# Performance work log

Measured on AMD Instinct MI355X. Metric: run time of the kernel, lower is better.

## Reference

```python
import jax, jax.numpy as jnp
import numpy as np

NEG_SLOPE = 0.2
LN_EPS = 1e-5


def _gat_layer(x, src, dst, W, a_src, a_dst, N):
    # x: [N, Fin], W: [Fin, H*C], a_src/a_dst: [H, C]
    H, C = a_src.shape
    h = (x @ W).reshape(N, H, C)
    al_src = (h * a_src).sum(-1)  # [N, H]
    al_dst = (h * a_dst).sum(-1)  # [N, H]
    e = jax.nn.leaky_relu(al_src[src] + al_dst[dst], NEG_SLOPE)  # [E, H]
    m = jax.ops.segment_max(e, dst, num_segments=N)
    e = jnp.exp(e - m[dst])
    denom = jax.ops.segment_sum(e, dst, num_segments=N)
    alpha = e / denom[dst]  # softmax over incoming edges per dst node
    msg = h[src] * alpha[:, :, None]  # [E, H, C]
    return jax.ops.segment_sum(msg, dst, num_segments=N)  # [N, H, C]


def _layer_norm(x, g, b):
    mu = x.mean(-1, keepdims=True)
    var = ((x - mu) ** 2).mean(-1, keepdims=True)
    return (x - mu) * jax.lax.rsqrt(var + LN_EPS) * g + b


def setup_inputs() -> dict:
    key = jax.random.key(0)
    ks = jax.random.split(key, 20)
    N, E, Fin, Ch, H = 50000, 800000, 128, 64, 4
    s = lambda k, shp, sc=0.05: jax.random.normal(k, shp, dtype=jnp.float32) * sc
    return {
        "x": jax.random.normal(ks[0], (N, Fin), dtype=jnp.float32),
        "edge_index": jax.random.randint(ks[1], (2, E), 0, N, dtype=jnp.int64),
        "W1": s(ks[2], (Fin, H * Ch)),
        "att_src1": s(ks[3], (H, Ch)),
        "att_dst1": s(ks[4], (H, Ch)),
        "b1": jnp.zeros((H * Ch,), jnp.float32),
        "ln1_g": jnp.ones((H * Ch,), jnp.float32),
        "ln1_b": jnp.zeros((H * Ch,), jnp.float32),
        "W2": s(ks[5], (H * Ch, Ch)),
        "att_src2": s(ks[6], (1, Ch)),
        "att_dst2": s(ks[7], (1, Ch)),
        "b2": jnp.zeros((Ch,), jnp.float32),
        "ln2_g": jnp.ones((Ch,), jnp.float32),
        "ln2_b": jnp.zeros((Ch,), jnp.float32),
        "fc1_W": s(ks[8], (Ch, Ch // 2)),
        "fc1_b": jnp.zeros((Ch // 2,), jnp.float32),
        "fc2_W": s(ks[9], (Ch // 2, 1)),
        "fc2_b": jnp.zeros((1,), jnp.float32),
    }


def reference(x, edge_index, W1, att_src1, att_dst1, b1, ln1_g, ln1_b,
              W2, att_src2, att_dst2, b2, ln2_g, ln2_b,
              fc1_W, fc1_b, fc2_W, fc2_b):
    N = x.shape[0]
    # PyG GATConv adds self-loops by default
    loop = jnp.arange(N, dtype=edge_index.dtype)
    src = jnp.concatenate([edge_index[0], loop])
    dst = jnp.concatenate([edge_index[1], loop])

    # GAT layer 1 (heads=4, concat) + LayerNorm + ReLU (dropout is identity in eval)
    h = _gat_layer(x, src, dst, W1, att_src1, att_dst1, N).reshape(N, -1) + b1
    h = jax.nn.relu(_layer_norm(h, ln1_g, ln1_b))

    # GAT layer 2 (heads=1) + LayerNorm + ReLU
    h = _gat_layer(h, src, dst, W2, att_src2, att_dst2, N).reshape(N, -1) + b2
    h = jax.nn.relu(_layer_norm(h, ln2_g, ln2_b))

    # MLP head
    h = jax.nn.relu(h @ fc1_W + fc1_b)
    return h @ fc2_W + fc2_b  # [N, 1]
```

## Files before the change

### kernel.cpp

```cpp
#include <hip/hip_runtime.h>
#include <hip/hip_fp16.h>
#include <math.h>

#define NEG_SLOPE 0.2f
#define LN_EPS 1e-5f
#define SCCHUNK 8192
#define PADCAP 64
#define CURPAD 32

typedef __attribute__((ext_vector_type(8))) _Float16 half8;
typedef __attribute__((ext_vector_type(4))) _Float16 half4;
typedef __attribute__((ext_vector_type(4))) float floatx4;

static __device__ __forceinline__ float lrelu(float e) {
    return e > 0.0f ? e : NEG_SLOPE * e;
}

__global__ __launch_bounds__(256) void k_g1sc(
    const float* __restrict__ x, const float* __restrict__ W1,
    const float* __restrict__ as1, const float* __restrict__ ad1,
    _Float16* __restrict__ h1, float* __restrict__ als, float* __restrict__ ald,
    const int* __restrict__ ei, unsigned* __restrict__ cursor,
    unsigned short* __restrict__ eidx,
    int N, int E, int nsc)
{
    const int tid = threadIdx.x;

    if ((int)blockIdx.x < nsc) {
        const unsigned basev = cursor[(size_t)N * CURPAD];
        const int Et = E + N;
        const int i0 = blockIdx.x * SCCHUNK;
#pragma unroll 4
        for (int j = 0; j < SCCHUNK / 256; ++j) {
            int i = i0 + j * 256 + tid;
            if (i < Et) {
                int s, d;
                if (i < E) { s = ei[i]; d = ei[E + i]; } else { s = d = i - E; }
                unsigned pos = atomicAdd(&cursor[(size_t)d * CURPAD], 1u) - basev;
                if (pos < PADCAP) eidx[(size_t)d * PADCAP + pos] = (unsigned short)s;
            }
        }
        return;
    }

    const int tile = blockIdx.x - nsc;
    const int lane = tid & 63, w = tid >> 6;
    const int l15 = lane & 15, quad = lane >> 4;
    const int r_base = tile * 64;

    half8 B[4][4];
    float asv[4], adv[4];
#pragma unroll
    for (int nt = 0; nt < 4; ++nt) {
        const int n = w * 64 + nt * 16 + l15;
        asv[nt] = as1[n]; adv[nt] = ad1[n];
#pragma unroll
        for (int ks = 0; ks < 4; ++ks) {
            const int k0 = ks * 32 + quad * 8;
            half8 b;
#pragma unroll
            for (int j = 0; j < 8; ++j) b[j] = (_Float16)W1[(size_t)(k0 + j) * 256 + n];
            B[ks][nt] = b;
        }
    }

#pragma unroll
    for (int rt = 0; rt < 4; ++rt) {
        const int r0 = r_base + rt * 16;
        int m = r0 + l15; if (m >= N) m = N - 1;
        half8 A[4];
#pragma unroll
        for (int ks = 0; ks < 4; ++ks) {
            const int k0 = ks * 32 + quad * 8;
            const float4* xp = (const float4*)(x + (size_t)m * 128 + k0);
            float4 v0 = xp[0], v1 = xp[1];
            half8 a;
            a[0] = (_Float16)v0.x; a[1] = (_Float16)v0.y; a[2] = (_Float16)v0.z; a[3] = (_Float16)v0.w;
            a[4] = (_Float16)v1.x; a[5] = (_Float16)v1.y; a[6] = (_Float16)v1.z; a[7] = (_Float16)v1.w;
            A[ks] = a;
        }
        floatx4 C[4];
#pragma unroll
        for (int nt = 0; nt < 4; ++nt) C[nt] = (floatx4){0.f, 0.f, 0.f, 0.f};
#pragma unroll
        for (int ks = 0; ks < 4; ++ks)
#pragma unroll
            for (int nt = 0; nt < 4; ++nt)
                C[nt] = __builtin_amdgcn_mfma_f32_16x16x32_f16(A[ks], B[ks][nt], C[nt], 0, 0, 0);

#pragma unroll
        for (int reg = 0; reg < 4; ++reg) {
            const int row = r0 + quad * 4 + reg;
            float vs = 0.f, vd = 0.f;
#pragma unroll
            for (int nt = 0; nt < 4; ++nt) {
                float c = C[nt][reg];
                if (row < N) h1[(size_t)row * 256 + w * 64 + nt * 16 + l15] = (_Float16)c;
                vs += c * asv[nt]; vd += c * adv[nt];
            }
#pragma unroll
            for (int o = 1; o < 16; o <<= 1) { vs += __shfl_xor(vs, o); vd += __shfl_xor(vd, o); }
            if (l15 == 0 && row < N) { als[row * 4 + w] = vs; ald[row * 4 + w] = vd; }
        }
    }
}

__global__ __launch_bounds__(256) void k_agg1(
    const _Float16* __restrict__ h1, const float* __restrict__ als, const float* __restrict__ ald,
    const unsigned* __restrict__ cursor, const unsigned short* __restrict__ eidx,
    const float* __restrict__ b1, const float* __restrict__ g1, const float* __restrict__ be1,
    _Float16* __restrict__ hln1, int N)
{
    __shared__ float alp[4][64][4];
    const int wv = threadIdx.x >> 6, lane = threadIdx.x & 63;
    int n = blockIdx.x * 4 + wv;
    if (n >= N) n = N - 1;
    const int base = n * PADCAP;
    const unsigned basev = cursor[(size_t)N * CURPAD];
    int deg = (int)(cursor[(size_t)n * CURPAD] - basev); if (deg > PADCAP) deg = PADCAP;
    const float4 ad = ((const float4*)ald)[n];

    const int srcv = eidx[base + (lane < deg ? lane : deg - 1)];
    float e0 = -1e30f, e1 = -1e30f, e2 = -1e30f, e3 = -1e30f;
    if (lane < deg) {
        float4 a4 = ((const float4*)als)[srcv];
        e0 = lrelu(a4.x + ad.x);
        e1 = lrelu(a4.y + ad.y);
        e2 = lrelu(a4.z + ad.z);
        e3 = lrelu(a4.w + ad.w);
    }
    float m0 = e0, m1 = e1, m2 = e2, m3 = e3;
#pragma unroll
    for (int o = 32; o; o >>= 1) {
        m0 = fmaxf(m0, __shfl_xor(m0, o));
        m1 = fmaxf(m1, __shfl_xor(m1, o));
        m2 = fmaxf(m2, __shfl_xor(m2, o));
        m3 = fmaxf(m3, __shfl_xor(m3, o));
    }
    float p0 = __expf(e0 - m0), p1 = __expf(e1 - m1);
    float p2 = __expf(e2 - m2), p3 = __expf(e3 - m3);
    float s0 = p0, s1 = p1, s2 = p2, s3 = p3;
#pragma unroll
    for (int o = 32; o; o >>= 1) {
        s0 += __shfl_xor(s0, o);
        s1 += __shfl_xor(s1, o);
        s2 += __shfl_xor(s2, o);
        s3 += __shfl_xor(s3, o);
    }
    float4 av;
    av.x = p0 / s0; av.y = p1 / s1; av.z = p2 / s2; av.w = p3 / s3;
    *(float4*)(&alp[wv][lane][0]) = av;

    float4 acc = make_float4(0.f, 0.f, 0.f, 0.f);
    const int hd = lane >> 4;
    const float* alpr = &alp[wv][0][hd];
    const int degr = (deg + 7) & ~7;
    for (int eb = 0; eb < degr; eb += 8) {
#pragma unroll
        for (int u = 0; u < 8; ++u) {
            const int e = eb + u;
            int s = __builtin_amdgcn_readlane(srcv, e);
            float a_e = alpr[e * 4];
            half4 v = *(const half4*)(h1 + (size_t)s * 256 + 4 * lane);
            acc.x = fmaf((float)v.x, a_e, acc.x);
            acc.y = fmaf((float)v.y, a_e, acc.y);
            acc.z = fmaf((float)v.z, a_e, acc.z);
            acc.w = fmaf((float)v.w, a_e, acc.w);
        }
    }

    float4 bb = ((const float4*)b1)[lane];
    float y0 = acc.x + bb.x, y1 = acc.y + bb.y, y2 = acc.z + bb.z, y3 = acc.w + bb.w;
    float ps = y0 + y1 + y2 + y3;
    float pss = y0 * y0 + y1 * y1 + y2 * y2 + y3 * y3;
#pragma unroll
    for (int o = 32; o; o >>= 1) { ps += __shfl_xor(ps, o); pss += __shfl_xor(pss, o); }
    float mu = ps * (1.f / 256.f);
    float var = pss * (1.f / 256.f) - mu * mu;
    float rstd = rsqrtf(var + LN_EPS);
    float4 gg = ((const float4*)g1)[lane];
    float4 b2v = ((const float4*)be1)[lane];
    half4 outv;
    outv.x = (_Float16)fmaxf((y0 - mu) * rstd * gg.x + b2v.x, 0.f);
    outv.y = (_Float16)fmaxf((y1 - mu) * rstd * gg.y + b2v.y, 0.f);
    outv.z = (_Float16)fmaxf((y2 - mu) * rstd * gg.z + b2v.z, 0.f);
    outv.w = (_Float16)fmaxf((y3 - mu) * rstd * gg.w + b2v.w, 0.f);
    ((half4*)(hln1 + (size_t)n * 256))[lane] = outv;
}

__global__ __launch_bounds__(256) void k_gemm2(
    const _Float16* __restrict__ hln1, const float* __restrict__ W2,
    const float* __restrict__ as2, const float* __restrict__ ad2,
    _Float16* __restrict__ h2, float* __restrict__ als2, float* __restrict__ ald2, int N)
{
    __shared__ float ps_s[4][64], ps_d[4][64];
    const int lane = threadIdx.x & 63, w = threadIdx.x >> 6;
    const int l15 = lane & 15, quad = lane >> 4;
    const int r_base = blockIdx.x * 64;

    const int n = w * 16 + l15;
    const float asv = as2[n], adv = ad2[n];
    half8 B[8];
#pragma unroll
    for (int ks = 0; ks < 8; ++ks) {
        const int k0 = ks * 32 + quad * 8;
        half8 b;
#pragma unroll
        for (int j = 0; j < 8; ++j) b[j] = (_Float16)W2[(size_t)(k0 + j) * 64 + n];
        B[ks] = b;
    }

#pragma unroll
    for (int rt = 0; rt < 4; ++rt) {
        const int r0 = r_base + rt * 16;
        int m = r0 + l15; if (m >= N) m = N - 1;
        floatx4 C = (floatx4){0.f, 0.f, 0.f, 0.f};
#pragma unroll
        for (int ks = 0; ks < 8; ++ks) {
            half8 a = *(const half8*)(hln1 + (size_t)m * 256 + ks * 32 + quad * 8);
            C = __builtin_amdgcn_mfma_f32_16x16x32_f16(a, B[ks], C, 0, 0, 0);
        }
#pragma unroll
        for (int reg = 0; reg < 4; ++reg) {
            const int row = r0 + quad * 4 + reg;
            float c = C[reg];
            if (row < N) h2[(size_t)row * 64 + n] = (_Float16)c;
            float vs = c * asv, vd = c * adv;
#pragma unroll
            for (int o = 1; o < 16; o <<= 1) { vs += __shfl_xor(vs, o); vd += __shfl_xor(vd, o); }
            if (l15 == 0) {
                ps_s[w][rt * 16 + quad * 4 + reg] = vs;
                ps_d[w][rt * 16 + quad * 4 + reg] = vd;
            }
        }
    }
    __syncthreads();
    const int t = threadIdx.x;
    if (t < 64) {
        const int row = r_base + t;
        if (row < N) {
            als2[row] = ps_s[0][t] + ps_s[1][t] + ps_s[2][t] + ps_s[3][t];
            ald2[row] = ps_d[0][t] + ps_d[1][t] + ps_d[2][t] + ps_d[3][t];
        }
    }
}

__global__ __launch_bounds__(256) void k_agg2(
    const _Float16* __restrict__ h2, const float* __restrict__ als, const float* __restrict__ ald,
    const unsigned* __restrict__ cursor, const unsigned short* __restrict__ eidx,
    const float* __restrict__ b2, const float* __restrict__ g2, const float* __restrict__ be2,
    const float* __restrict__ fc1W, const float* __restrict__ fc1b,
    const float* __restrict__ fc2W, const float* __restrict__ fc2b,
    float* __restrict__ out, int N)
{
    __shared__ float sh[4][64];
    const int wv = threadIdx.x >> 6, lane = threadIdx.x & 63;
    int n = blockIdx.x * 4 + wv;
    if (n >= N) n = N - 1;
    const int base = n * PADCAP;
    const unsigned basev = cursor[(size_t)N * CURPAD];
    int deg = (int)(cursor[(size_t)n * CURPAD] - basev); if (deg > PADCAP) deg = PADCAP;
    const float adn = ald[n];

    const int srcv = eidx[base + (lane < deg ? lane : deg - 1)];
    float e = -1e30f;
    if (lane < deg) e = lrelu(als[srcv] + adn);
    float m = e;
#pragma unroll
    for (int o = 32; o; o >>= 1) m = fmaxf(m, __shfl_xor(m, o));
    float p = __expf(e - m);
    float s = p;
#pragma unroll
    for (int o = 32; o; o >>= 1) s += __shfl_xor(s, o);
    const float alpha = p / s;

    float acc = 0.f;
    const int degr = (deg + 7) & ~7;
    for (int eb = 0; eb < degr; eb += 8) {
#pragma unroll
        for (int u = 0; u < 8; ++u) {
            const int e2 = eb + u;
            int sidx = __builtin_amdgcn_readlane(srcv, e2);
            float a_e = __int_as_float(
                __builtin_amdgcn_readlane(__float_as_int(alpha), e2));
            acc = fmaf((float)h2[(size_t)sidx * 64 + lane], a_e, acc);
        }
    }

    float y = acc + b2[lane];
    float ps = y, pss = y * y;
#pragma unroll
    for (int o = 32; o; o >>= 1) { ps += __shfl_xor(ps, o); pss += __shfl_xor(pss, o); }
    float mu = ps * (1.f / 64.f);
    float var = pss * (1.f / 64.f) - mu * mu;
    float r = fmaxf((y - mu) * rsqrtf(var + LN_EPS) * g2[lane] + be2[lane], 0.f);

    sh[wv][lane] = r;

    if (lane < 32) {
        float a1 = fc1b[lane];
#pragma unroll 8
        for (int k = 0; k < 64; ++k) a1 += sh[wv][k] * fc1W[k * 32 + lane];
        a1 = fmaxf(a1, 0.f);
        float t = a1 * fc2W[lane];
#pragma unroll
        for (int o = 16; o; o >>= 1) t += __shfl_xor(t, o);
        if (lane == 0) out[n] = t + fc2b[0];
    }
}

extern "C" void kernel_launch(void* const* d_in, const int* in_sizes, int n_in,
                              void* d_out, int out_size, void* d_ws, size_t ws_size,
                              hipStream_t stream)
{
    const float* x   = (const float*)d_in[0];
    const int* ei    = (const int*)d_in[1];
    const float* W1  = (const float*)d_in[2];
    const float* as1 = (const float*)d_in[3];
    const float* ad1 = (const float*)d_in[4];
    const float* b1  = (const float*)d_in[5];
    const float* g1  = (const float*)d_in[6];
    const float* be1 = (const float*)d_in[7];
    const float* W2  = (const float*)d_in[8];
    const float* as2 = (const float*)d_in[9];
    const float* ad2 = (const float*)d_in[10];
    const float* b2  = (const float*)d_in[11];
    const float* g2  = (const float*)d_in[12];
    const float* be2 = (const float*)d_in[13];
    const float* fc1W = (const float*)d_in[14];
    const float* fc1b = (const float*)d_in[15];
    const float* fc2W = (const float*)d_in[16];
    const float* fc2b = (const float*)d_in[17];
    float* out = (float*)d_out;

    const int N = in_sizes[0] / 128;
    const int E = in_sizes[1] / 2;
    const int Et = E + N;
    const int nsc = (Et + SCCHUNK - 1) / SCCHUNK;
    const int ntiles = (N + 63) / 64;

    char* p = (char*)d_ws;
    auto carve = [&](size_t bytes) {
        void* q = p;
        p += (bytes + 255) & ~(size_t)255;
        return q;
    };
    _Float16* h1    = (_Float16*)carve((size_t)N * 256 * 2);
    _Float16* hln1h = (_Float16*)carve((size_t)N * 256 * 2);
    _Float16* h2    = (_Float16*)carve((size_t)N * 64 * 2);
    float* als1 = (float*)carve((size_t)N * 4 * 4);
    float* ald1 = (float*)carve((size_t)N * 4 * 4);
    float* als2 = (float*)carve((size_t)N * 4);
    float* ald2 = (float*)carve((size_t)N * 4);
    unsigned* cursor = (unsigned*)carve((size_t)(N + 1) * CURPAD * 4);
    unsigned short* eidx = (unsigned short*)carve((size_t)N * PADCAP * 2);

    k_g1sc<<<nsc + ntiles, 256, 0, stream>>>(x, W1, as1, ad1, h1, als1, ald1,
                                             ei, cursor, eidx, N, E, nsc);
    k_agg1<<<(N + 3) / 4, 256, 0, stream>>>(h1, als1, ald1, cursor, eidx, b1, g1, be1, hln1h, N);
    k_gemm2<<<(N + 63) / 64, 256, 0, stream>>>(hln1h, W2, as2, ad2, h2, als2, ald2, N);
    k_agg2<<<(N + 3) / 4, 256, 0, stream>>>(h2, als2, ald2, cursor, eidx,
                                            b2, g2, be2, fc1W, fc1b, fc2W, fc2b, out, N);
}
```

Measured before the change: 277.4 us.

## Split fused scatter/GEMM1 kernel and batch scatter loads and atomics

The combined kernel that did edge scattering in some blocks and the layer-1 GEMM in others is split into two separate launches. The scatter kernel now loads all 32 edges per thread first, then issues all atomics, then all stores, so many memory operations are in flight at once instead of a serialized load-atomic-store chain. This costs an extra launch and loses the concurrent overlap of scatter and GEMM blocks within one grid, and it raises register pressure in the scatter kernel.

```diff
diff --git a/kernel.cpp b/kernel.cpp
--- a/kernel.cpp
+++ b/kernel.cpp
@@ -16,37 +16,52 @@
     return e > 0.0f ? e : NEG_SLOPE * e;
 }
 
-__global__ __launch_bounds__(256) void k_g1sc(
+__global__ __launch_bounds__(256) void k_scatter(
+    const int* __restrict__ ei, unsigned* __restrict__ cursor,
+    unsigned short* __restrict__ eidx, int N, int E)
+{
+    const int tid = threadIdx.x;
+    const unsigned basev = cursor[(size_t)N * CURPAD];
+    const int Et = E + N;
+    const int i0 = blockIdx.x * SCCHUNK;
+
+    int s[32], d[32];
+    unsigned pos[32];
+
+#pragma unroll
+    for (int j = 0; j < 32; ++j) {
+        const int i = i0 + j * 256 + tid;
+        if (i < Et) {
+            if (i < E) { s[j] = ei[i]; d[j] = ei[E + i]; }
+            else       { s[j] = d[j] = i - E; }
+        } else {
+            d[j] = -1;
+        }
+    }
+#pragma unroll
+    for (int j = 0; j < 32; ++j) {
+        if (d[j] >= 0)
+            pos[j] = atomicAdd(&cursor[(size_t)d[j] * CURPAD], 1u);
+    }
+#pragma unroll
+    for (int j = 0; j < 32; ++j) {
+        if (d[j] >= 0) {
+            unsigned p = pos[j] - basev;
+            if (p < PADCAP) eidx[(size_t)d[j] * PADCAP + p] = (unsigned short)s[j];
+        }
+    }
+}
+
+__global__ __launch_bounds__(256) void k_gemm1(
     const float* __restrict__ x, const float* __restrict__ W1,
     const float* __restrict__ as1, const float* __restrict__ ad1,
     _Float16* __restrict__ h1, float* __restrict__ als, float* __restrict__ ald,
-    const int* __restrict__ ei, unsigned* __restrict__ cursor,
-    unsigned short* __restrict__ eidx,
-    int N, int E, int nsc)
+    int N)
 {
     const int tid = threadIdx.x;
-
-    if ((int)blockIdx.x < nsc) {
-        const unsigned basev = cursor[(size_t)N * CURPAD];
-        const int Et = E + N;
-        const int i0 = blockIdx.x * SCCHUNK;
-#pragma unroll 4
-        for (int j = 0; j < SCCHUNK / 256; ++j) {
-            int i = i0 + j * 256 + tid;
-            if (i < Et) {
-                int s, d;
-                if (i < E) { s = ei[i]; d = ei[E + i]; } else { s = d = i - E; }
-                unsigned pos = atomicAdd(&cursor[(size_t)d * CURPAD], 1u) - basev;
-                if (pos < PADCAP) eidx[(size_t)d * PADCAP + pos] = (unsigned short)s;
-            }
-        }
-        return;
-    }
-
-    const int tile = blockIdx.x - nsc;
     const int lane = tid & 63, w = tid >> 6;
     const int l15 = lane & 15, quad = lane >> 4;
-    const int r_base = tile * 64;
+    const int r_base = blockIdx.x * 64;
 
     half8 B[4][4];
     float asv[4], adv[4];
@@ -355,8 +370,8 @@
     unsigned* cursor = (unsigned*)carve((size_t)(N + 1) * CURPAD * 4);
     unsigned short* eidx = (unsigned short*)carve((size_t)N * PADCAP * 2);
 
-    k_g1sc<<<nsc + ntiles, 256, 0, stream>>>(x, W1, as1, ad1, h1, als1, ald1,
-                                             ei, cursor, eidx, N, E, nsc);
+    k_scatter<<<nsc, 256, 0, stream>>>(ei, cursor, eidx, N, E);
+    k_gemm1<<<ntiles, 256, 0, stream>>>(x, W1, as1, ad1, h1, als1, ald1, N);
     k_agg1<<<(N + 3) / 4, 256, 0, stream>>>(h1, als1, ald1, cursor, eidx, b1, g1, be1, hln1h, N);
     k_gemm2<<<(N + 63) / 64, 256, 0, stream>>>(hln1h, W2, as2, ad2, h2, als2, ald2, N);
     k_agg2<<<(N + 3) / 4, 256, 0, stream>>>(h2, als2, ald2, cursor, eidx,
```

Result: slower. 307.1 us (+10.7%).

## Widen gather loads in GAT aggregation kernels, splitting edges across lane groups

Applied to the files above, without the earlier changes.

Both aggregation kernels now gather feature rows with wider per-lane loads: 16-byte half8 in layer 1 and half4 in layer 2. Each wave splits edges across lane groups (two halves or four quarters) and combines the partial sums with cross-lane shuffles. Source indices and attention weights are staged in shared memory and no longer broadcast with readlane. The aim is fewer, wider gather instructions and more edges in flight per iteration. The cost is extra shuffle reductions, shared-memory traffic, and the LayerNorm statistics being reduced over duplicated lanes (hence the adjusted divisors).

```diff
diff --git a/kernel.cpp b/kernel.cpp
--- a/kernel.cpp
+++ b/kernel.cpp
@@ -112,6 +112,7 @@
     _Float16* __restrict__ hln1, int N)
 {
     __shared__ float alp[4][64][4];
+    __shared__ int   srcl[4][64];
     const int wv = threadIdx.x >> 6, lane = threadIdx.x & 63;
     int n = blockIdx.x * 4 + wv;
     if (n >= N) n = N - 1;
@@ -150,42 +151,61 @@
     float4 av;
     av.x = p0 / s0; av.y = p1 / s1; av.z = p2 / s2; av.w = p3 / s3;
     *(float4*)(&alp[wv][lane][0]) = av;
-
-    float4 acc = make_float4(0.f, 0.f, 0.f, 0.f);
-    const int hd = lane >> 4;
-    const float* alpr = &alp[wv][0][hd];
+    srcl[wv][lane] = srcv;
+
+    const int half_ = lane >> 5, l31 = lane & 31, hd = l31 >> 3;
+    float4 a0 = make_float4(0.f, 0.f, 0.f, 0.f);
+    float4 a1 = make_float4(0.f, 0.f, 0.f, 0.f);
     const int degr = (deg + 7) & ~7;
     for (int eb = 0; eb < degr; eb += 8) {
 #pragma unroll
-        for (int u = 0; u < 8; ++u) {
-            const int e = eb + u;
-            int s = __builtin_amdgcn_readlane(srcv, e);
-            float a_e = alpr[e * 4];
-            half4 v = *(const half4*)(h1 + (size_t)s * 256 + 4 * lane);
-            acc.x = fmaf((float)v.x, a_e, acc.x);
-            acc.y = fmaf((float)v.y, a_e, acc.y);
-            acc.z = fmaf((float)v.z, a_e, acc.z);
-            acc.w = fmaf((float)v.w, a_e, acc.w);
-        }
-    }
-
-    float4 bb = ((const float4*)b1)[lane];
-    float y0 = acc.x + bb.x, y1 = acc.y + bb.y, y2 = acc.z + bb.z, y3 = acc.w + bb.w;
-    float ps = y0 + y1 + y2 + y3;
-    float pss = y0 * y0 + y1 * y1 + y2 * y2 + y3 * y3;
+        for (int u = 0; u < 4; ++u) {
+            const int e = eb + 2 * u + half_;
+            int s = srcl[wv][e];
+            float ae = alp[wv][e][hd];
+            half8 v = *(const half8*)(h1 + (size_t)s * 256 + l31 * 8);
+            a0.x = fmaf((float)v[0], ae, a0.x);
+            a0.y = fmaf((float)v[1], ae, a0.y);
+            a0.z = fmaf((float)v[2], ae, a0.z);
+            a0.w = fmaf((float)v[3], ae, a0.w);
+            a1.x = fmaf((float)v[4], ae, a1.x);
+            a1.y = fmaf((float)v[5], ae, a1.y);
+            a1.z = fmaf((float)v[6], ae, a1.z);
+            a1.w = fmaf((float)v[7], ae, a1.w);
+        }
+    }
+    a0.x += __shfl_xor(a0.x, 32); a0.y += __shfl_xor(a0.y, 32);
+    a0.z += __shfl_xor(a0.z, 32); a0.w += __shfl_xor(a0.w, 32);
+    a1.x += __shfl_xor(a1.x, 32); a1.y += __shfl_xor(a1.y, 32);
+    a1.z += __shfl_xor(a1.z, 32); a1.w += __shfl_xor(a1.w, 32);
+
+    const float4 bb0 = ((const float4*)b1)[l31 * 2];
+    const float4 bb1 = ((const float4*)b1)[l31 * 2 + 1];
+    float y0 = a0.x + bb0.x, y1 = a0.y + bb0.y, y2 = a0.z + bb0.z, y3 = a0.w + bb0.w;
+    float y4 = a1.x + bb1.x, y5 = a1.y + bb1.y, y6 = a1.z + bb1.z, y7 = a1.w + bb1.w;
+    float ps  = y0 + y1 + y2 + y3 + y4 + y5 + y6 + y7;
+    float pss = y0*y0 + y1*y1 + y2*y2 + y3*y3 + y4*y4 + y5*y5 + y6*y6 + y7*y7;
 #pragma unroll
     for (int o = 32; o; o >>= 1) { ps += __shfl_xor(ps, o); pss += __shfl_xor(pss, o); }
-    float mu = ps * (1.f / 256.f);
-    float var = pss * (1.f / 256.f) - mu * mu;
+    float mu = ps * (1.f / 512.f);
+    float var = pss * (1.f / 512.f) - mu * mu;
     float rstd = rsqrtf(var + LN_EPS);
-    float4 gg = ((const float4*)g1)[lane];
-    float4 b2v = ((const float4*)be1)[lane];
-    half4 outv;
-    outv.x = (_Float16)fmaxf((y0 - mu) * rstd * gg.x + b2v.x, 0.f);
-    outv.y = (_Float16)fmaxf((y1 - mu) * rstd * gg.y + b2v.y, 0.f);
-    outv.z = (_Float16)fmaxf((y2 - mu) * rstd * gg.z + b2v.z, 0.f);
-    outv.w = (_Float16)fmaxf((y3 - mu) * rstd * gg.w + b2v.w, 0.f);
-    ((half4*)(hln1 + (size_t)n * 256))[lane] = outv;
+    const float4 gg0 = ((const float4*)g1)[l31 * 2];
+    const float4 gg1 = ((const float4*)g1)[l31 * 2 + 1];
+    const float4 be0 = ((const float4*)be1)[l31 * 2];
+    const float4 be1v = ((const float4*)be1)[l31 * 2 + 1];
+    if (lane < 32) {
+        half8 outv;
+        outv[0] = (_Float16)fmaxf((y0 - mu) * rstd * gg0.x + be0.x, 0.f);
+        outv[1] = (_Float16)fmaxf((y1 - mu) * rstd * gg0.y + be0.y, 0.f);
+        outv[2] = (_Float16)fmaxf((y2 - mu) * rstd * gg0.z + be0.z, 0.f);
+        outv[3] = (_Float16)fmaxf((y3 - mu) * rstd * gg0.w + be0.w, 0.f);
+        outv[4] = (_Float16)fmaxf((y4 - mu) * rstd * gg1.x + be1v.x, 0.f);
+        outv[5] = (_Float16)fmaxf((y5 - mu) * rstd * gg1.y + be1v.y, 0.f);
+        outv[6] = (_Float16)fmaxf((y6 - mu) * rstd * gg1.z + be1v.z, 0.f);
+        outv[7] = (_Float16)fmaxf((y7 - mu) * rstd * gg1.w + be1v.w, 0.f);
+        *(half8*)(hln1 + (size_t)n * 256 + l31 * 8) = outv;
+    }
 }
 
 __global__ __launch_bounds__(256) void k_gemm2(
@@ -254,6 +274,8 @@
     float* __restrict__ out, int N)
 {
     __shared__ float sh[4][64];
+    __shared__ float alp2[4][64];
+    __shared__ int   src2[4][64];
     const int wv = threadIdx.x >> 6, lane = threadIdx.x & 63;
     int n = blockIdx.x * 4 + wv;
     if (n >= N) n = N - 1;
@@ -272,30 +294,49 @@
     float s = p;
 #pragma unroll
     for (int o = 32; o; o >>= 1) s += __shfl_xor(s, o);
-    const float alpha = p / s;
-
-    float acc = 0.f;
+    alp2[wv][lane] = p / s;
+    src2[wv][lane] = srcv;
+
+    const int grp = lane >> 4, l15 = lane & 15;
+    float4 acc = make_float4(0.f, 0.f, 0.f, 0.f);
     const int degr = (deg + 7) & ~7;
     for (int eb = 0; eb < degr; eb += 8) {
 #pragma unroll
-        for (int u = 0; u < 8; ++u) {
-            const int e2 = eb + u;
-            int sidx = __builtin_amdgcn_readlane(srcv, e2);
-            float a_e = __int_as_float(
-                __builtin_amdgcn_readlane(__float_as_int(alpha), e2));
-            acc = fmaf((float)h2[(size_t)sidx * 64 + lane], a_e, acc);
-        }
-    }
-
-    float y = acc + b2[lane];
-    float ps = y, pss = y * y;
+        for (int u = 0; u < 2; ++u) {
+            const int e2 = eb + 4 * u + grp;
+            int sidx = src2[wv][e2];
+            float a_e = alp2[wv][e2];
+            half4 v = *(const half4*)(h2 + (size_t)sidx * 64 + l15 * 4);
+            acc.x = fmaf((float)v.x, a_e, acc.x);
+            acc.y = fmaf((float)v.y, a_e, acc.y);
+            acc.z = fmaf((float)v.z, a_e, acc.z);
+            acc.w = fmaf((float)v.w, a_e, acc.w);
+        }
+    }
+    acc.x += __shfl_xor(acc.x, 16); acc.y += __shfl_xor(acc.y, 16);
+    acc.z += __shfl_xor(acc.z, 16); acc.w += __shfl_xor(acc.w, 16);
+    acc.x += __shfl_xor(acc.x, 32); acc.y += __shfl_xor(acc.y, 32);
+    acc.z += __shfl_xor(acc.z, 32); acc.w += __shfl_xor(acc.w, 32);
+
+    const float4 bb = ((const float4*)b2)[l15];
+    float y0 = acc.x + bb.x, y1 = acc.y + bb.y, y2 = acc.z + bb.z, y3 = acc.w + bb.w;
+    float ps = y0 + y1 + y2 + y3;
+    float pss = y0*y0 + y1*y1 + y2*y2 + y3*y3;
 #pragma unroll
     for (int o = 32; o; o >>= 1) { ps += __shfl_xor(ps, o); pss += __shfl_xor(pss, o); }
-    float mu = ps * (1.f / 64.f);
-    float var = pss * (1.f / 64.f) - mu * mu;
-    float r = fmaxf((y - mu) * rsqrtf(var + LN_EPS) * g2[lane] + be2[lane], 0.f);
-
-    sh[wv][lane] = r;
+    float mu = ps * (1.f / 256.f);
+    float var = pss * (1.f / 256.f) - mu * mu;
+    float rstd = rsqrtf(var + LN_EPS);
+    const float4 gg = ((const float4*)g2)[l15];
+    const float4 bev = ((const float4*)be2)[l15];
+    if (grp == 0) {
+        float4 r;
+        r.x = fmaxf((y0 - mu) * rstd * gg.x + bev.x, 0.f);
+        r.y = fmaxf((y1 - mu) * rstd * gg.y + bev.y, 0.f);
+        r.z = fmaxf((y2 - mu) * rstd * gg.z + bev.z, 0.f);
+        r.w = fmaxf((y3 - mu) * rstd * gg.w + bev.w, 0.f);
+        *(float4*)(&sh[wv][l15 * 4]) = r;
+    }
 
     if (lane < 32) {
         float a1 = fc1b[lane];
```

New measurement: 285.7 us. 3.0% more time.

## Fuse all four GAT stages into one persistent cooperative kernel with grid syncs

Applied to the files above, without the earlier changes.

Replaces the four separate kernel launches with a single cooperative persistent kernel. It uses grid-stride loops for the GEMM, aggregation and head stages, separated by grid.sync barriers. The aim is to remove launch overhead and inter-kernel gaps. In exchange, the grid is capped by occupancy (6 blocks/CU via launch bounds), which may reduce latency hiding in the memory-bound gather stages and adds grid-barrier cost.

```diff
diff --git a/kernel.cpp b/kernel.cpp
--- a/kernel.cpp
+++ b/kernel.cpp
@@ -1,6 +1,9 @@
 #include <hip/hip_runtime.h>
 #include <hip/hip_fp16.h>
+#include <hip/hip_cooperative_groups.h>
 #include <math.h>
+
+namespace cg = cooperative_groups;
 
 #define NEG_SLOPE 0.2f
 #define LN_EPS 1e-5f
@@ -16,20 +19,38 @@
     return e > 0.0f ? e : NEG_SLOPE * e;
 }
 
-__global__ __launch_bounds__(256) void k_g1sc(
-    const float* __restrict__ x, const float* __restrict__ W1,
-    const float* __restrict__ as1, const float* __restrict__ ad1,
-    _Float16* __restrict__ h1, float* __restrict__ als, float* __restrict__ ald,
-    const int* __restrict__ ei, unsigned* __restrict__ cursor,
-    unsigned short* __restrict__ eidx,
-    int N, int E, int nsc)
+__global__ __launch_bounds__(256, 6) void k_fused(
+    const float* __restrict__ x, const int* __restrict__ ei,
+    const float* __restrict__ W1, const float* __restrict__ as1, const float* __restrict__ ad1,
+    const float* __restrict__ b1, const float* __restrict__ g1, const float* __restrict__ be1,
+    const float* __restrict__ W2, const float* __restrict__ as2, const float* __restrict__ ad2,
+    const float* __restrict__ b2, const float* __restrict__ g2, const float* __restrict__ be2,
+    const float* __restrict__ fc1W, const float* __restrict__ fc1b,
+    const float* __restrict__ fc2W, const float* __restrict__ fc2b,
+    float* __restrict__ out,
+    _Float16* __restrict__ h1, _Float16* __restrict__ hln1, _Float16* __restrict__ h2,
+    float* __restrict__ als1, float* __restrict__ ald1,
+    float* __restrict__ als2, float* __restrict__ ald2,
+    unsigned* __restrict__ cursor, unsigned short* __restrict__ eidx,
+    int N, int E, int nsc, int ntiles, int nagg)
 {
+    cg::grid_group grid = cg::this_grid();
     const int tid = threadIdx.x;
-
-    if ((int)blockIdx.x < nsc) {
-        const unsigned basev = cursor[(size_t)N * CURPAD];
+    const int bid = blockIdx.x;
+    const int G = gridDim.x;
+    const int lane = tid & 63, wv = tid >> 6;
+    const int l15 = lane & 15, quad = lane >> 4;
+
+    __shared__ float s_alp[4][64][4];
+    __shared__ float s_ps[2][4][64];
+    __shared__ float s_sh[4][64];
+
+    const unsigned basev = cursor[(size_t)N * CURPAD];
+
+    if (bid >= G - nsc) {
+        const int chunk = bid - (G - nsc);
         const int Et = E + N;
-        const int i0 = blockIdx.x * SCCHUNK;
+        const int i0 = chunk * SCCHUNK;
 #pragma unroll 4
         for (int j = 0; j < SCCHUNK / 256; ++j) {
             int i = i0 + j * 256 + tid;
@@ -40,272 +61,246 @@
                 if (pos < PADCAP) eidx[(size_t)d * PADCAP + pos] = (unsigned short)s;
             }
         }
-        return;
-    }
-
-    const int tile = blockIdx.x - nsc;
-    const int lane = tid & 63, w = tid >> 6;
-    const int l15 = lane & 15, quad = lane >> 4;
-    const int r_base = tile * 64;
-
-    half8 B[4][4];
-    float asv[4], adv[4];
-#pragma unroll
-    for (int nt = 0; nt < 4; ++nt) {
-        const int n = w * 64 + nt * 16 + l15;
-        asv[nt] = as1[n]; adv[nt] = ad1[n];
-#pragma unroll
-        for (int ks = 0; ks < 4; ++ks) {
+    } else {
+        half8 B[4][4];
+        float asv[4], adv[4];
+#pragma unroll
+        for (int nt = 0; nt < 4; ++nt) {
+            const int n = wv * 64 + nt * 16 + l15;
+            asv[nt] = as1[n]; adv[nt] = ad1[n];
+#pragma unroll
+            for (int ks = 0; ks < 4; ++ks) {
+                const int k0 = ks * 32 + quad * 8;
+                half8 b;
+#pragma unroll
+                for (int j = 0; j < 8; ++j) b[j] = (_Float16)W1[(size_t)(k0 + j) * 256 + n];
+                B[ks][nt] = b;
+            }
+        }
+        for (int tile = bid; tile < ntiles; tile += (G - nsc)) {
+            const int r_base = tile * 64;
+#pragma unroll
+            for (int rt = 0; rt < 4; ++rt) {
+                const int r0 = r_base + rt * 16;
+                int m = r0 + l15; if (m >= N) m = N - 1;
+                half8 A[4];
+#pragma unroll
+                for (int ks = 0; ks < 4; ++ks) {
+                    const int k0 = ks * 32 + quad * 8;
+                    const float4* xp = (const float4*)(x + (size_t)m * 128 + k0);
+                    float4 v0 = xp[0], v1 = xp[1];
+                    half8 a;
+                    a[0] = (_Float16)v0.x; a[1] = (_Float16)v0.y; a[2] = (_Float16)v0.z; a[3] = (_Float16)v0.w;
+                    a[4] = (_Float16)v1.x; a[5] = (_Float16)v1.y; a[6] = (_Float16)v1.z; a[7] = (_Float16)v1.w;
+                    A[ks] = a;
+                }
+                floatx4 C[4];
+#pragma unroll
+                for (int nt = 0; nt < 4; ++nt) C[nt] = (floatx4){0.f, 0.f, 0.f, 0.f};
+#pragma unroll
+                for (int ks = 0; ks < 4; ++ks)
+#pragma unroll
+                    for (int nt = 0; nt < 4; ++nt)
+                        C[nt] = __builtin_amdgcn_mfma_f32_16x16x32_f16(A[ks], B[ks][nt], C[nt], 0, 0, 0);
+
+#pragma unroll
+                for (int reg = 0; reg < 4; ++reg) {
+                    const int row = r0 + quad * 4 + reg;
+                    float vs = 0.f, vd = 0.f;
+#pragma unroll
+                    for (int nt = 0; nt < 4; ++nt) {
+                        float c = C[nt][reg];
+                        if (row < N) h1[(size_t)row * 256 + wv * 64 + nt * 16 + l15] = (_Float16)c;
+                        vs += c * asv[nt]; vd += c * adv[nt];
+                    }
+#pragma unroll
+                    for (int o = 1; o < 16; o <<= 1) { vs += __shfl_xor(vs, o); vd += __shfl_xor(vd, o); }
+                    if (l15 == 0 && row < N) { als1[row * 4 + wv] = vs; ald1[row * 4 + wv] = vd; }
+                }
+            }
+        }
+    }
+    grid.sync();
+
+    for (int blk = bid; blk < nagg; blk += G) {
+        int n = blk * 4 + wv;
+        if (n >= N) n = N - 1;
+        const int base = n * PADCAP;
+        int deg = (int)(cursor[(size_t)n * CURPAD] - basev); if (deg > PADCAP) deg = PADCAP;
+        const float4 ad = ((const float4*)ald1)[n];
+
+        const int srcv = eidx[base + (lane < deg ? lane : deg - 1)];
+        float e0 = -1e30f, e1 = -1e30f, e2 = -1e30f, e3 = -1e30f;
+        if (lane < deg) {
+            float4 a4 = ((const float4*)als1)[srcv];
+            e0 = lrelu(a4.x + ad.x);
+            e1 = lrelu(a4.y + ad.y);
+            e2 = lrelu(a4.z + ad.z);
+            e3 = lrelu(a4.w + ad.w);
+        }
+        float m0 = e0, m1 = e1, m2 = e2, m3 = e3;
+#pragma unroll
+        for (int o = 32; o; o >>= 1) {
+            m0 = fmaxf(m0, __shfl_xor(m0, o));
+            m1 = fmaxf(m1, __shfl_xor(m1, o));
+            m2 = fmaxf(m2, __shfl_xor(m2, o));
+            m3 = fmaxf(m3, __shfl_xor(m3, o));
+        }
+        float p0 = __expf(e0 - m0), p1 = __expf(e1 - m1);
+        float p2 = __expf(e2 - m2), p3 = __expf(e3 - m3);
+        float s0 = p0, s1 = p1, s2 = p2, s3 = p3;
+#pragma unroll
+        for (int o = 32; o; o >>= 1) {
+            s0 += __shfl_xor(s0, o);
+            s1 += __shfl_xor(s1, o);
+            s2 += __shfl_xor(s2, o);
+            s3 += __shfl_xor(s3, o);
+        }
+        float4 av;
+        av.x = p0 / s0; av.y = p1 / s1; av.z = p2 / s2; av.w = p3 / s3;
+        *(float4*)(&s_alp[wv][lane][0]) = av;
+
+        float4 acc = make_float4(0.f, 0.f, 0.f, 0.f);
+        const int hd = lane >> 4;
+        const float* alpr = &s_alp[wv][0][hd];
+        const int degr = (deg + 7) & ~7;
+        for (int eb = 0; eb < degr; eb += 8) {
+#pragma unroll
+            for (int u = 0; u < 8; ++u) {
+                const int e = eb + u;
+                int s = __builtin_amdgcn_readlane(srcv, e);
+                float a_e = alpr[e * 4];
+                half4 v = *(const half4*)(h1 + (size_t)s * 256 + 4 * lane);
+                acc.x = fmaf((float)v.x, a_e, acc.x);
+                acc.y = fmaf((float)v.y, a_e, acc.y);
+                acc.z = fmaf((float)v.z, a_e, acc.z);
+                acc.w = fmaf((float)v.w, a_e, acc.w);
+            }
+        }
+
+        float4 bb = ((const float4*)b1)[lane];
+        float y0 = acc.x + bb.x, y1 = acc.y + bb.y, y2 = acc.z + bb.z, y3 = acc.w + bb.w;
+        float ps = y0 + y1 + y2 + y3;
+        float pss = y0 * y0 + y1 * y1 + y2 * y2 + y3 * y3;
+#pragma unroll
+        for (int o = 32; o; o >>= 1) { ps += __shfl_xor(ps, o); pss += __shfl_xor(pss, o); }
+        float mu = ps * (1.f / 256.f);
+        float var = pss * (1.f / 256.f) - mu * mu;
+        float rstd = rsqrtf(var + LN_EPS);
+        float4 gg = ((const float4*)g1)[lane];
+        float4 b2v = ((const float4*)be1)[lane];
+        half4 outv;
+        outv.x = (_Float16)fmaxf((y0 - mu) * rstd * gg.x + b2v.x, 0.f);
+        outv.y = (_Float16)fmaxf((y1 - mu) * rstd * gg.y + b2v.y, 0.f);
+        outv.z = (_Float16)fmaxf((y2 - mu) * rstd * gg.z + b2v.z, 0.f);
+        outv.w = (_Float16)fmaxf((y3 - mu) * rstd * gg.w + b2v.w, 0.f);
+        ((half4*)(hln1 + (size_t)n * 256))[lane] = outv;
+    }
+    grid.sync();
+
+    {
+        const int n = wv * 16 + l15;
+        const float asv = as2[n], adv = ad2[n];
+        half8 B[8];
+#pragma unroll
+        for (int ks = 0; ks < 8; ++ks) {
             const int k0 = ks * 32 + quad * 8;
             half8 b;
 #pragma unroll
-            for (int j = 0; j < 8; ++j) b[j] = (_Float16)W1[(size_t)(k0 + j) * 256 + n];
-            B[ks][nt] = b;
-        }
-    }
-
-#pragma unroll
-    for (int rt = 0; rt < 4; ++rt) {
-        const int r0 = r_base + rt * 16;
-        int m = r0 + l15; if (m >= N) m = N - 1;
-        half8 A[4];
-#pragma unroll
-        for (int ks = 0; ks < 4; ++ks) {
-            const int k0 = ks * 32 + quad * 8;
-            const float4* xp = (const float4*)(x + (size_t)m * 128 + k0);
-            float4 v0 = xp[0], v1 = xp[1];
-            half8 a;
-            a[0] = (_Float16)v0.x; a[1] = (_Float16)v0.y; a[2] = (_Float16)v0.z; a[3] = (_Float16)v0.w;
-            a[4] = (_Float16)v1.x; a[5] = (_Float16)v1.y; a[6] = (_Float16)v1.z; a[7] = (_Float16)v1.w;
-            A[ks] = a;
-        }
-        floatx4 C[4];
-#pragma unroll
-        for (int nt = 0; nt < 4; ++nt) C[nt] = (floatx4){0.f, 0.f, 0.f, 0.f};
-#pragma unroll
-        for (int ks = 0; ks < 4; ++ks)
-#pragma unroll
-            for (int nt = 0; nt < 4; ++nt)
-                C[nt] = __builtin_amdgcn_mfma_f32_16x16x32_f16(A[ks], B[ks][nt], C[nt], 0, 0, 0);
-
-#pragma unroll
-        for (int reg = 0; reg < 4; ++reg) {
-            const int row = r0 + quad * 4 + reg;
-            float vs = 0.f, vd = 0.f;
-#pragma unroll
-            for (int nt = 0; nt < 4; ++nt) {
-                float c = C[nt][reg];
-                if (row < N) h1[(size_t)row * 256 + w * 64 + nt * 16 + l15] = (_Float16)c;
-                vs += c * asv[nt]; vd += c * adv[nt];
-            }
-#pragma unroll
-            for (int o = 1; o < 16; o <<= 1) { vs += __shfl_xor(vs, o); vd += __shfl_xor(vd, o); }
-            if (l15 == 0 && row < N) { als[row * 4 + w] = vs; ald[row * 4 + w] = vd; }
-        }
-    }
-}
-
-__global__ __launch_bounds__(256) void k_agg1(
-    const _Float16* __restrict__ h1, const float* __restrict__ als, const float* __restrict__ ald,
-    const unsigned* __restrict__ cursor, const unsigned short* __restrict__ eidx,
-    const float* __restrict__ b1, const float* __restrict__ g1, const float* __restrict__ be1,
-    _Float16* __restrict__ hln1, int N)
-{
-    __shared__ float alp[4][64][4];
-    const int wv = threadIdx.x >> 6, lane = threadIdx.x & 63;
-    int n = blockIdx.x * 4 + wv;
-    if (n >= N) n = N - 1;
-    const int base = n * PADCAP;
-    const unsigned basev = cursor[(size_t)N * CURPAD];
-    int deg = (int)(cursor[(size_t)n * CURPAD] - basev); if (deg > PADCAP) deg = PADCAP;
-    const float4 ad = ((const float4*)ald)[n];
-
-    const int srcv = eidx[base + (lane < deg ? lane : deg - 1)];
-    float e0 = -1e30f, e1 = -1e30f, e2 = -1e30f, e3 = -1e30f;
-    if (lane < deg) {
-        float4 a4 = ((const float4*)als)[srcv];
-        e0 = lrelu(a4.x + ad.x);
-        e1 = lrelu(a4.y + ad.y);
-        e2 = lrelu(a4.z + ad.z);
-        e3 = lrelu(a4.w + ad.w);
-    }
-    float m0 = e0, m1 = e1, m2 = e2, m3 = e3;
-#pragma unroll
-    for (int o = 32; o; o >>= 1) {
-        m0 = fmaxf(m0, __shfl_xor(m0, o));
-        m1 = fmaxf(m1, __shfl_xor(m1, o));
-        m2 = fmaxf(m2, __shfl_xor(m2, o));
-        m3 = fmaxf(m3, __shfl_xor(m3, o));
-    }
-    float p0 = __expf(e0 - m0), p1 = __expf(e1 - m1);
-    float p2 = __expf(e2 - m2), p3 = __expf(e3 - m3);
-    float s0 = p0, s1 = p1, s2 = p2, s3 = p3;
-#pragma unroll
-    for (int o = 32; o; o >>= 1) {
-        s0 += __shfl_xor(s0, o);
-        s1 += __shfl_xor(s1, o);
-        s2 += __shfl_xor(s2, o);
-        s3 += __shfl_xor(s3, o);
-    }
-    float4 av;
-    av.x = p0 / s0; av.y = p1 / s1; av.z = p2 / s2; av.w = p3 / s3;
-    *(float4*)(&alp[wv][lane][0]) = av;
-
-    float4 acc = make_float4(0.f, 0.f, 0.f, 0.f);
-    const int hd = lane >> 4;
-    const float* alpr = &alp[wv][0][hd];
-    const int degr = (deg + 7) & ~7;
-    for (int eb = 0; eb < degr; eb += 8) {
-#pragma unroll
-        for (int u = 0; u < 8; ++u) {
-            const int e = eb + u;
-            int s = __builtin_amdgcn_readlane(srcv, e);
-            float a_e = alpr[e * 4];
-            half4 v = *(const half4*)(h1 + (size_t)s * 256 + 4 * lane);
-            acc.x = fmaf((float)v.x, a_e, acc.x);
-            acc.y = fmaf((float)v.y, a_e, acc.y);
-            acc.z = fmaf((float)v.z, a_e, acc.z);
-            acc.w = fmaf((float)v.w, a_e, acc.w);
-        }
-    }
-
-    float4 bb = ((const float4*)b1)[lane];
-    float y0 = acc.x + bb.x, y1 = acc.y + bb.y, y2 = acc.z + bb.z, y3 = acc.w + bb.w;
-    float ps = y0 + y1 + y2 + y3;
-    float pss = y0 * y0 + y1 * y1 + y2 * y2 + y3 * y3;
-#pragma unroll
-    for (int o = 32; o; o >>= 1) { ps += __shfl_xor(ps, o); pss += __shfl_xor(pss, o); }
-    float mu = ps * (1.f / 256.f);
-    float var = pss * (1.f / 256.f) - mu * mu;
-    float rstd = rsqrtf(var + LN_EPS);
-    float4 gg = ((const float4*)g1)[lane];
-    float4 b2v = ((const float4*)be1)[lane];
-    half4 outv;
-    outv.x = (_Float16)fmaxf((y0 - mu) * rstd * gg.x + b2v.x, 0.f);
-    outv.y = (_Float16)fmaxf((y1 - mu) * rstd * gg.y + b2v.y, 0.f);
-    outv.z = (_Float16)fmaxf((y2 - mu) * rstd * gg.z + b2v.z, 0.f);
-    outv.w = (_Float16)fmaxf((y3 - mu) * rstd * gg.w + b2v.w, 0.f);
-    ((half4*)(hln1 + (size_t)n * 256))[lane] = outv;
-}
-
-__global__ __launch_bounds__(256) void k_gemm2(
-    const _Float16* __restrict__ hln1, const float* __restrict__ W2,
-    const float* __restrict__ as2, const float* __restrict__ ad2,
-    _Float16* __restrict__ h2, float* __restrict__ als2, float* __restrict__ ald2, int N)
-{
-    __shared__ float ps_s[4][64], ps_d[4][64];
-    const int lane = threadIdx.x & 63, w = threadIdx.x >> 6;
-    const int l15 = lane & 15, quad = lane >> 4;
-    const int r_base = blockIdx.x * 64;
-
-    const int n = w * 16 + l15;
-    const float asv = as2[n], adv = ad2[n];
-    half8 B[8];
-#pragma unroll
-    for (int ks = 0; ks < 8; ++ks) {
-        const int k0 = ks * 32 + quad * 8;
-        half8 b;
-#pragma unroll
-        for (int j = 0; j < 8; ++j) b[j] = (_Float16)W2[(size_t)(k0 + j) * 64 + n];
-        B[ks] = b;
-    }
-
-#pragma unroll
-    for (int rt = 0; rt < 4; ++rt) {
-        const int r0 = r_base + rt * 16;
-        int m = r0 + l15; if (m >= N) m = N - 1;
-        floatx4 C = (floatx4){0.f, 0.f, 0.f, 0.f};
-#pragma unroll
-        for (int ks = 0; ks < 8; ++ks) {
-            half8 a = *(const half8*)(hln1 + (size_t)m * 256 + ks * 32 + quad * 8);
-            C = __builtin_amdgcn_mfma_f32_16x16x32_f16(a, B[ks], C, 0, 0, 0);
-        }
-#pragma unroll
-        for (int reg = 0; reg < 4; ++reg) {
-            const int row = r0 + quad * 4 + reg;
-            float c = C[reg];
-            if (row < N) h2[(size_t)row * 64 + n] = (_Float16)c;
-            float vs = c * asv, vd = c * adv;
-#pragma unroll
-            for (int o = 1; o < 16; o <<= 1) { vs += __shfl_xor(vs, o); vd += __shfl_xor(vd, o); }
-            if (l15 == 0) {
-                ps_s[w][rt * 16 + quad * 4 + reg] = vs;
-                ps_d[w][rt * 16 + quad * 4 + reg] = vd;
-            }
-        }
-    }
-    __syncthreads();
-    const int t = threadIdx.x;
-    if (t < 64) {
-        const int row = r_base + t;
-        if (row < N) {
-            als2[row] = ps_s[0][t] + ps_s[1][t] + ps_s[2][t] + ps_s[3][t];
-            ald2[row] = ps_d[0][t] + ps_d[1][t] + ps_d[2][t] + ps_d[3][t];
-        }
-    }
-}
-
-__global__ __launch_bounds__(256) void k_agg2(
-    const _Float16* __restrict__ h2, const float* __restrict__ als, const float* __restrict__ ald,
-    const unsigned* __restrict__ cursor, const unsigned short* __restrict__ eidx,
-    const float* __restrict__ b2, const float* __restrict__ g2, const float* __restrict__ be2,
-    const float* __restrict__ fc1W, const float* __restrict__ fc1b,
-    const float* __restrict__ fc2W, const float* __restrict__ fc2b,
-    float* __restrict__ out, int N)
-{
-    __shared__ float sh[4][64];
-    const int wv = threadIdx.x >> 6, lane = threadIdx.x & 63;
-    int n = blockIdx.x * 4 + wv;
-    if (n >= N) n = N - 1;
-    const int base = n * PADCAP;
-    const unsigned basev = cursor[(size_t)N * CURPAD];
-    int deg = (int)(cursor[(size_t)n * CURPAD] - basev); if (deg > PADCAP) deg = PADCAP;
-    const float adn = ald[n];
-
-    const int srcv = eidx[base + (lane < deg ? lane : deg - 1)];
-    float e = -1e30f;
-    if (lane < deg) e = lrelu(als[srcv] + adn);
-    float m = e;
-#pragma unroll
-    for (int o = 32; o; o >>= 1) m = fmaxf(m, __shfl_xor(m, o));
-    float p = __expf(e - m);
-    float s = p;
-#pragma unroll
-    for (int o = 32; o; o >>= 1) s += __shfl_xor(s, o);
-    const float alpha = p / s;
-
-    float acc = 0.f;
-    const int degr = (deg + 7) & ~7;
-    for (int eb = 0; eb < degr; eb += 8) {
-#pragma unroll
-        for (int u = 0; u < 8; ++u) {
-            const int e2 = eb + u;
-            int sidx = __builtin_amdgcn_readlane(srcv, e2);
-            float a_e = __int_as_float(
-                __builtin_amdgcn_readlane(__float_as_int(alpha), e2));
-            acc = fmaf((float)h2[(size_t)sidx * 64 + lane], a_e, acc);
-        }
-    }
-
-    float y = acc + b2[lane];
-    float ps = y, pss = y * y;
-#pragma unroll
-    for (int o = 32; o; o >>= 1) { ps += __shfl_xor(ps, o); pss += __shfl_xor(pss, o); }
-    float mu = ps * (1.f / 64.f);
-    float var = pss * (1.f / 64.f) - mu * mu;
-    float r = fmaxf((y - mu) * rsqrtf(var + LN_EPS) * g2[lane] + be2[lane], 0.f);
-
-    sh[wv][lane] = r;
-
-    if (lane < 32) {
-        float a1 = fc1b[lane];
+            for (int j = 0; j < 8; ++j) b[j] = (_Float16)W2[(size_t)(k0 + j) * 64 + n];
+            B[ks] = b;
+        }
+        for (int tile = bid; tile < ntiles; tile += G) {
+            const int r_base = tile * 64;
+#pragma unroll
+            for (int rt = 0; rt < 4; ++rt) {
+                const int r0 = r_base + rt * 16;
+                int m = r0 + l15; if (m >= N) m = N - 1;
+                floatx4 C = (floatx4){0.f, 0.f, 0.f, 0.f};
+#pragma unroll
+                for (int ks = 0; ks < 8; ++ks) {
+                    half8 a = *(const half8*)(hln1 + (size_t)m * 256 + ks * 32 + quad * 8);
+                    C = __builtin_amdgcn_mfma_f32_16x16x32_f16(a, B[ks], C, 0, 0, 0);
+                }
+#pragma unroll
+                for (int reg = 0; reg < 4; ++reg) {
+                    const int row = r0 + quad * 4 + reg;
+                    float c = C[reg];
+                    if (row < N) h2[(size_t)row * 64 + n] = (_Float16)c;
+                    float vs = c * asv, vd = c * adv;
+#pragma unroll
+                    for (int o = 1; o < 16; o <<= 1) { vs += __shfl_xor(vs, o); vd += __shfl_xor(vd, o); }
+                    if (l15 == 0) {
+                        s_ps[0][wv][rt * 16 + quad * 4 + reg] = vs;
+                        s_ps[1][wv][rt * 16 + quad * 4 + reg] = vd;
+                    }
+                }
+            }
+            __syncthreads();
+            if (tid < 64) {
+                const int row = r_base + tid;
+                if (row < N) {
+                    als2[row] = s_ps[0][0][tid] + s_ps[0][1][tid] + s_ps[0][2][tid] + s_ps[0][3][tid];
+                    ald2[row] = s_ps[1][0][tid] + s_ps[1][1][tid] + s_ps[1][2][tid] + s_ps[1][3][tid];
+                }
+            }
+            __syncthreads();
+        }
+    }
+    grid.sync();
+
+    for (int blk = bid; blk < nagg; blk += G) {
+        int n = blk * 4 + wv;
+        if (n >= N) n = N - 1;
+        const int base = n * PADCAP;
+        int deg = (int)(cursor[(size_t)n * CURPAD] - basev); if (deg > PADCAP) deg = PADCAP;
+        const float adn = ald2[n];
+
+        const int srcv = eidx[base + (lane < deg ? lane : deg - 1)];
+        float e = -1e30f;
+        if (lane < deg) e = lrelu(als2[srcv] + adn);
+        float m = e;
+#pragma unroll
+        for (int o = 32; o; o >>= 1) m = fmaxf(m, __shfl_xor(m, o));
+        float p = __expf(e - m);
+        float s = p;
+#pragma unroll
+        for (int o = 32; o; o >>= 1) s += __shfl_xor(s, o);
+        const float alpha = p / s;
+
+        float acc = 0.f;
+        const int degr = (deg + 7) & ~7;
+        for (int eb = 0; eb < degr; eb += 8) {
+#pragma unroll
+            for (int u = 0; u < 8; ++u) {
+                const int e2 = eb + u;
+                int sidx = __builtin_amdgcn_readlane(srcv, e2);
+                float a_e = __int_as_float(
+                    __builtin_amdgcn_readlane(__float_as_int(alpha), e2));
+                acc = fmaf((float)h2[(size_t)sidx * 64 + lane], a_e, acc);
+            }
+        }
+
+        float y = acc + b2[lane];
+        float ps = y, pss = y * y;
+#pragma unroll
+        for (int o = 32; o; o >>= 1) { ps += __shfl_xor(ps, o); pss += __shfl_xor(pss, o); }
+        float mu = ps * (1.f / 64.f);
+        float var = pss * (1.f / 64.f) - mu * mu;
+        float r = fmaxf((y - mu) * rsqrtf(var + LN_EPS) * g2[lane] + be2[lane], 0.f);
+
+        s_sh[wv][lane] = r;
+
+        if (lane < 32) {
+            float a1 = fc1b[lane];
 #pragma unroll 8
-        for (int k = 0; k < 64; ++k) a1 += sh[wv][k] * fc1W[k * 32 + lane];
-        a1 = fmaxf(a1, 0.f);
-        float t = a1 * fc2W[lane];
-#pragma unroll
-        for (int o = 16; o; o >>= 1) t += __shfl_xor(t, o);
-        if (lane == 0) out[n] = t + fc2b[0];
+            for (int k = 0; k < 64; ++k) a1 += s_sh[wv][k] * fc1W[k * 32 + lane];
+            a1 = fmaxf(a1, 0.f);
+            float t = a1 * fc2W[lane];
+#pragma unroll
+            for (int o = 16; o; o >>= 1) t += __shfl_xor(t, o);
+            if (lane == 0) out[n] = t + fc2b[0];
+        }
     }
 }
 
@@ -333,11 +328,12 @@
     const float* fc2b = (const float*)d_in[17];
     float* out = (float*)d_out;
 
-    const int N = in_sizes[0] / 128;
-    const int E = in_sizes[1] / 2;
+    int N = in_sizes[0] / 128;
+    int E = in_sizes[1] / 2;
     const int Et = E + N;
-    const int nsc = (Et + SCCHUNK - 1) / SCCHUNK;
-    const int ntiles = (N + 63) / 64;
+    int nsc = (Et + SCCHUNK - 1) / SCCHUNK;
+    int ntiles = (N + 63) / 64;
+    int nagg = (N + 3) / 4;
 
     char* p = (char*)d_ws;
     auto carve = [&](size_t bytes) {
@@ -346,7 +342,7 @@
         return q;
     };
     _Float16* h1    = (_Float16*)carve((size_t)N * 256 * 2);
-    _Float16* hln1h = (_Float16*)carve((size_t)N * 256 * 2);
+    _Float16* hln1  = (_Float16*)carve((size_t)N * 256 * 2);
     _Float16* h2    = (_Float16*)carve((size_t)N * 64 * 2);
     float* als1 = (float*)carve((size_t)N * 4 * 4);
     float* ald1 = (float*)carve((size_t)N * 4 * 4);
@@ -355,10 +351,26 @@
     unsigned* cursor = (unsigned*)carve((size_t)(N + 1) * CURPAD * 4);
     unsigned short* eidx = (unsigned short*)carve((size_t)N * PADCAP * 2);
 
-    k_g1sc<<<nsc + ntiles, 256, 0, stream>>>(x, W1, as1, ad1, h1, als1, ald1,
-                                             ei, cursor, eidx, N, E, nsc);
-    k_agg1<<<(N + 3) / 4, 256, 0, stream>>>(h1, als1, ald1, cursor, eidx, b1, g1, be1, hln1h, N);
-    k_gemm2<<<(N + 63) / 64, 256, 0, stream>>>(hln1h, W2, as2, ad2, h2, als2, ald2, N);
-    k_agg2<<<(N + 3) / 4, 256, 0, stream>>>(h2, als2, ald2, cursor, eidx,
-                                            b2, g2, be2, fc1W, fc1b, fc2W, fc2b, out, N);
+    static int gblocks = 0;
+    if (gblocks == 0) {
+        int nb = 0;
+        hipError_t err = hipOccupancyMaxActiveBlocksPerMultiprocessor(&nb, k_fused, 256, 0);
+        if (err != hipSuccess || nb < 1) nb = 2;
+        if (nb > 6) nb = 6;
+        gblocks = nb * 256;
+        if (gblocks < nsc + 1) gblocks = nsc + 1;
+    }
+
+    void* args[] = {
+        (void*)&x, (void*)&ei, (void*)&W1, (void*)&as1, (void*)&ad1,
+        (void*)&b1, (void*)&g1, (void*)&be1, (void*)&W2, (void*)&as2, (void*)&ad2,
+        (void*)&b2, (void*)&g2, (void*)&be2, (void*)&fc1W, (void*)&fc1b,
+        (void*)&fc2W, (void*)&fc2b, (void*)&out,
+        (void*)&h1, (void*)&hln1, (void*)&h2,
+        (void*)&als1, (void*)&ald1, (void*)&als2, (void*)&ald2,
+        (void*)&cursor, (void*)&eidx,
+        (void*)&N, (void*)&E, (void*)&nsc, (void*)&ntiles, (void*)&nagg
+    };
+    hipLaunchCooperativeKernel((const void*)k_fused, dim3(gblocks), dim3(256),
+                               args, 0, stream);
 }
```

New measurement: 673.0 us. 143% more time.
